# Kernel tuning notes

Measured on AMD Instinct MI355X. Metric: run time of the kernel, lower is better.

The kernel has to match this reference:

```python
import jax, jax.numpy as jnp
import numpy as np

B, C, T, H, W, L = 4, 256, 8, 16, 16, 8
NO = 8                # num_offsets
D = C // NO           # per-head feature dim for offset/weight MLPs
EPS = 1e-5


def setup_inputs() -> dict:
    key = jax.random.key(0)
    ks = jax.random.split(key, 6)
    return {
        "features": jax.random.normal(ks[0], (B, C, T, H, W, L), jnp.float32),
        "pos": jax.random.normal(ks[1], (B, C, T, H, W, L), jnp.float32),
        "Wp": jax.random.normal(ks[2], (C, 3 * C), jnp.float32) * 0.02,  # 1x1x1 conv: 3C -> C
        "bp": jnp.zeros((C,), jnp.float32),
        "Wo": jax.random.normal(ks[3], (D, 3), jnp.float32) * 0.02,      # offset_embed Linear(d,3)
        "bo": jnp.zeros((3,), jnp.float32),
        "Ww": jax.random.normal(ks[4], (D, 2), jnp.float32) * 0.02,      # weight_embed Linear(d,2)
        "bw": jnp.zeros((2,), jnp.float32),
    }


def _trilinear_sample(feat, coords):
    """feat: (N,C,D1,D2,D3); coords: (N,G,3) in [-1,1] (axis order D1,D2,D3).
    align_corners=False, zeros padding (matches F.grid_sample semantics)."""
    N, Cc, D1, D2, D3 = feat.shape
    sizes = jnp.asarray([D1, D2, D3], feat.dtype)
    pix = ((coords + 1.0) * sizes - 1.0) * 0.5       # unnormalize to pixel coords
    lo = jnp.floor(pix)
    frac = pix - lo                                   # (N,G,3)
    lo = lo.astype(jnp.int32)
    dims = jnp.asarray([D1, D2, D3], jnp.int32)
    feat_flat = feat.reshape(N, Cc, D1 * D2 * D3)
    out = jnp.zeros((N, Cc, coords.shape[1]), feat.dtype)
    for dz in (0, 1):
        for dy in (0, 1):
            for dx in (0, 1):
                off = jnp.asarray([dz, dy, dx], jnp.int32)
                idx = lo + off                        # (N,G,3)
                wz = jnp.where(dz, frac[..., 0], 1.0 - frac[..., 0])
                wy = jnp.where(dy, frac[..., 1], 1.0 - frac[..., 1])
                wx = jnp.where(dx, frac[..., 2], 1.0 - frac[..., 2])
                wgt = wz * wy * wx                    # (N,G)
                valid = jnp.all((idx >= 0) & (idx < dims), axis=-1)
                idc = jnp.clip(idx, 0, dims - 1)
                lin = (idc[..., 0] * D2 + idc[..., 1]) * D3 + idc[..., 2]  # (N,G)
                vals = jnp.take_along_axis(feat_flat, lin[:, None, :], axis=2)  # (N,C,G)
                out = out + vals * (wgt * valid)[:, None, :]
    return out


def reference(features, pos, Wp, bp, Wo, bo, Ww, bw):
    Bv, Cv, Tv, Hv, Wv, Lv = features.shape
    BT = Bv * Tv
    feat = features.transpose(0, 2, 1, 3, 4, 5).reshape(BT, Cv, Hv, Wv, Lv)
    posr = pos.transpose(0, 2, 1, 3, 4, 5).reshape(BT, Cv, Hv, Wv, Lv)
    # global context + projection (1x1x1 conv over 3C channels) + ReLU
    glob = feat.mean(axis=(2, 3, 4), keepdims=True)
    src = jnp.concatenate([feat, posr, jnp.broadcast_to(glob, feat.shape)], axis=1)  # (BT,3C,H,W,L)
    proj = jax.nn.relu(jnp.einsum('nixyz,oi->noxyz', src, Wp) + bp[None, :, None, None, None])
    osrc = proj.transpose(0, 2, 3, 4, 1).reshape(BT, Hv, Wv, Lv, NO, D)
    # per-voxel per-head offsets in (0,1) and scalar weights
    offset = jax.nn.sigmoid(osrc @ Wo + bo)                      # (BT,H,W,L,NO,3)
    wgt = jax.nn.softmax(osrc @ Ww + bw, axis=-1)[..., 1]        # (BT,H,W,L,NO)
    # base flow field in [-1,1], deform in logit space, re-sigmoid
    base = jnp.stack(jnp.meshgrid(jnp.linspace(-1.0, 1.0, Hv),
                                  jnp.linspace(-1.0, 1.0, Wv),
                                  jnp.linspace(-1.0, 1.0, Lv), indexing='ij'), axis=-1)
    base01 = jnp.clip((base + 1.0) * 0.5, EPS, 1.0 - EPS)
    logit = jnp.log(base01 / (1.0 - base01))                     # (H,W,L,3)
    sp = jax.nn.sigmoid(logit[None, :, :, :, None, :] + offset)  # (BT,H,W,L,NO,3)
    grid = (sp * 2.0 - 1.0).transpose(0, 4, 1, 2, 3, 5).reshape(BT, NO * Hv * Wv * Lv, 3)
    sampled = _trilinear_sample(feat, grid).reshape(BT, Cv, NO, Hv, Wv, Lv)
    out = feat + jnp.einsum('bcnhwl,bhwln->bchwl', sampled, wgt)
    return out.reshape(Bv, Tv, Cv, Hv, Wv, Lv).transpose(0, 2, 1, 3, 4, 5)
```

## Files before the change

### kernel.cpp

```cpp
#include <hip/hip_runtime.h>

#define BB 4
#define CC 256
#define TT 8
#define HH 16
#define WW 16
#define LL 8
#define NO 8
#define DD 32
#define BT 32
#define VV 2048
#define KIN 512
#define EPS_ 1e-5f

typedef short bf16x8 __attribute__((ext_vector_type(8)));
typedef float f32x4 __attribute__((ext_vector_type(4)));

static __device__ __forceinline__ float b2f(unsigned short u) {
    return __uint_as_float(((unsigned int)u) << 16);
}
static __device__ __forceinline__ float b2f_lo(unsigned int x) {
    return __uint_as_float(x << 16);
}
static __device__ __forceinline__ float b2f_hi(unsigned int x) {
    return __uint_as_float(x & 0xffff0000u);
}
static __device__ __forceinline__ unsigned short f2b(float f) {
    unsigned int x = __float_as_uint(f);
    unsigned int r = x + 0x7fffu + ((x >> 16) & 1u);
    return (unsigned short)(r >> 16);
}
static __device__ __forceinline__ unsigned int f2b_pk(float lo, float hi) {
    return (unsigned int)f2b(lo) | ((unsigned int)f2b(hi) << 16);
}
static __device__ __forceinline__ float sigm(float x) {
    return 1.0f / (1.0f + __expf(-x));
}

__global__ __launch_bounds__(256) void k0_prep(const float* __restrict__ Wp,
                                               unsigned short* __restrict__ Wa,
                                               float* __restrict__ glob) {
    int i = blockIdx.x * 256 + threadIdx.x;
    if (i < CC * KIN) {
        int o = i >> 9, k = i & 511;
        Wa[i] = f2b(Wp[o * 768 + k]);
    } else if (i < CC * KIN + BT * CC) {
        glob[i - CC * KIN] = 0.0f;
    }
}

__global__ __launch_bounds__(256) void k1_transpose(const float* __restrict__ features,
                                                    const float* __restrict__ pos,
                                                    unsigned short* __restrict__ srcT,
                                                    float* __restrict__ glob) {
    const int n = blockIdx.x;
    const int v0 = blockIdx.y * 16;
    const int b = n >> 3, t = n & 7;
    const int tid = threadIdx.x;
    const int ty = tid >> 4;
    const int tx = tid & 15;

    __shared__ unsigned short s1[16 * 520];

    for (int cb = 0; cb < CC; cb += 16) {
        int c = cb + ty;
        size_t fidx = (((size_t)b * CC + c) * TT + t) * VV + v0 + tx;
        float f = features[fidx];
        float p = pos[fidx];
        s1[tx * 520 + c] = f2b(f);
        s1[tx * 520 + 256 + c] = f2b(p);
        for (int d = 8; d > 0; d >>= 1) f += __shfl_down(f, d, 16);
        if (tx == 0) atomicAdd(&glob[n * CC + c], f);
    }
    __syncthreads();
    const size_t base = ((size_t)n * VV + v0) * KIN;
    for (int q = tid; q < 1024; q += 256) {
        int row = q >> 6;
        int koff = (q & 63) * 8;
        *(uint4*)&srcT[base + (size_t)row * KIN + koff] = *(const uint4*)&s1[row * 520 + koff];
    }
}

__global__ __launch_bounds__(256) void k2_gterm(const float* __restrict__ glob,
                                                const float* __restrict__ Wp,
                                                const float* __restrict__ bp,
                                                float* __restrict__ gterm) {
    const int n = blockIdx.x;
    const int o = threadIdx.x;
    __shared__ float gl[CC];
    gl[o] = glob[n * CC + o] * (1.0f / (float)VV);
    __syncthreads();
    const float4* wrow = (const float4*)(Wp + (size_t)o * 768 + 512);
    const float4* g4 = (const float4*)gl;
    float s = bp[o];
    #pragma unroll 8
    for (int c = 0; c < 64; ++c) {
        float4 w = wrow[c], g = g4[c];
        s += w.x * g.x + w.y * g.y + w.z * g.z + w.w * g.w;
    }
    gterm[n * CC + o] = s;
}

__global__ __launch_bounds__(256) void k3_gemm(const unsigned short* __restrict__ Wa,
                                               const unsigned short* __restrict__ srcT,
                                               const float* __restrict__ gterm,
                                               unsigned short* __restrict__ projT) {
    const int n  = blockIdx.x;
    const int mb = blockIdx.y;
    const int nb = blockIdx.z;
    const int tid = threadIdx.x;
    const int m0 = mb * 128, v0 = nb * 128;

    __shared__ short As[128 * 40];
    __shared__ short Bs[128 * 40];

    const int wv = tid >> 6;
    const int lane = tid & 63;
    const int wm = wv >> 1, wn = wv & 1;
    const int lr = lane & 15, lq = lane >> 4;

    f32x4 acc[4][4];
    #pragma unroll
    for (int i = 0; i < 4; ++i)
        #pragma unroll
        for (int j = 0; j < 4; ++j)
            acc[i][j] = (f32x4){0.f, 0.f, 0.f, 0.f};

    const int row = tid >> 1, half = tid & 1;
    const unsigned short* agp = Wa + (size_t)(m0 + row) * KIN + half * 16;
    const unsigned short* bgp = srcT + ((size_t)n * VV + v0 + row) * KIN + half * 16;
    short* asp = &As[row * 40 + half * 16];
    short* bsp = &Bs[row * 40 + half * 16];

    for (int k0 = 0; k0 < KIN; k0 += 32) {
        uint4 a0 = *(const uint4*)(agp + k0);
        uint4 a1 = *(const uint4*)(agp + k0 + 8);
        uint4 b0 = *(const uint4*)(bgp + k0);
        uint4 b1 = *(const uint4*)(bgp + k0 + 8);
        __syncthreads();
        *(uint4*)asp = a0; *(uint4*)(asp + 8) = a1;
        *(uint4*)bsp = b0; *(uint4*)(bsp + 8) = b1;
        __syncthreads();

        bf16x8 af[4], bf[4];
        #pragma unroll
        for (int i = 0; i < 4; ++i)
            af[i] = *(const bf16x8*)&As[(wm * 64 + i * 16 + lr) * 40 + lq * 8];
        #pragma unroll
        for (int j = 0; j < 4; ++j)
            bf[j] = *(const bf16x8*)&Bs[(wn * 64 + j * 16 + lr) * 40 + lq * 8];
        #pragma unroll
        for (int i = 0; i < 4; ++i)
            #pragma unroll
            for (int j = 0; j < 4; ++j)
                acc[i][j] = __builtin_amdgcn_mfma_f32_16x16x32_bf16(af[i], bf[j], acc[i][j], 0, 0, 0);
    }

    #pragma unroll
    for (int i = 0; i < 4; ++i) {
        const int og = m0 + wm * 64 + i * 16 + lq * 4;
        float4 g = *(const float4*)(gterm + n * CC + og);
        #pragma unroll
        for (int j = 0; j < 4; ++j) {
            const int vg = v0 + wn * 64 + j * 16 + lr;
            float x0 = fmaxf(acc[i][j][0] + g.x, 0.0f);
            float x1 = fmaxf(acc[i][j][1] + g.y, 0.0f);
            float x2 = fmaxf(acc[i][j][2] + g.z, 0.0f);
            float x3 = fmaxf(acc[i][j][3] + g.w, 0.0f);
            ushort4 st;
            st.x = f2b(x0); st.y = f2b(x1); st.z = f2b(x2); st.w = f2b(x3);
            *(ushort4*)&projT[((size_t)n * VV + vg) * CC + og] = st;
        }
    }
}

__global__ __launch_bounds__(256) void k4_coef(const unsigned short* __restrict__ projT,
                                               const float* __restrict__ Wo,
                                               const float* __restrict__ bo,
                                               const float* __restrict__ Ww,
                                               const float* __restrict__ bw,
                                               int2* __restrict__ pairs) {
    __shared__ float sWo[96], sWw[64], sb[5];
    const int tid = threadIdx.x;
    if (tid < 96) sWo[tid] = Wo[tid];
    if (tid < 64) sWw[tid] = Ww[tid];
    if (tid < 3)  sb[tid] = bo[tid];
    if (tid < 2)  sb[3 + tid] = bw[tid];
    __syncthreads();

    const int g = blockIdx.x * 256 + tid;
    const int n = g >> 14;
    const int rem = g & 16383;
    const int v = rem >> 3;
    const int hd = rem & 7;

    const uint4* up = (const uint4*)(projT + ((size_t)n * VV + v) * CC + hd * DD);
    float osrc[32];
    #pragma unroll
    for (int q = 0; q < 4; ++q) {
        uint4 u = up[q];
        unsigned int ws4[4] = {u.x, u.y, u.z, u.w};
        #pragma unroll
        for (int e = 0; e < 4; ++e) {
            osrc[q * 8 + e * 2]     = b2f_lo(ws4[e]);
            osrc[q * 8 + e * 2 + 1] = b2f_hi(ws4[e]);
        }
    }

    float o0 = sb[0], o1 = sb[1], o2 = sb[2];
    float zw = sb[4] - sb[3];
    #pragma unroll
    for (int d = 0; d < DD; ++d) {
        float t = osrc[d];
        o0 += t * sWo[3 * d + 0];
        o1 += t * sWo[3 * d + 1];
        o2 += t * sWo[3 * d + 2];
        zw += t * (sWw[2 * d + 1] - sWw[2 * d]);
    }
    const float wgt = sigm(zw);

    const int h = v >> 7, w = (v >> 3) & 15, l = v & 7;
    float ph = fminf(fmaxf(h * (1.0f / 15.0f), EPS_), 1.0f - EPS_);
    float pw = fminf(fmaxf(w * (1.0f / 15.0f), EPS_), 1.0f - EPS_);
    float pl = fminf(fmaxf(l * (1.0f / 7.0f),  EPS_), 1.0f - EPS_);
    float lh = __logf(ph / (1.0f - ph));
    float lw = __logf(pw / (1.0f - pw));
    float ll = __logf(pl / (1.0f - pl));

    float sph = sigm(lh + sigm(o0));
    float spw = sigm(lw + sigm(o1));
    float spl = sigm(ll + sigm(o2));
    float pixh = sph * 16.0f - 0.5f;
    float pixw = spw * 16.0f - 0.5f;
    float pixl = spl * 8.0f  - 0.5f;

    float flh = floorf(pixh), flw = floorf(pixw), fll = floorf(pixl);
    float fh = pixh - flh, fw = pixw - flw, fl = pixl - fll;
    int ih = (int)flh, iw = (int)flw, il = (int)fll;

    int2* pp = pairs + (size_t)g * 8;
    #pragma unroll
    for (int dz = 0; dz < 2; ++dz)
        #pragma unroll
        for (int dy = 0; dy < 2; ++dy)
            #pragma unroll
            for (int dx = 0; dx < 2; ++dx) {
                int iz = ih + dz, iy = iw + dy, ix = il + dx;
                float wt = (dz ? fh : 1.0f - fh) * (dy ? fw : 1.0f - fw) * (dx ? fl : 1.0f - fl) * wgt;
                bool valid = ((unsigned)iz < 16u) && ((unsigned)iy < 16u) && ((unsigned)ix < 8u);
                int lin = valid ? ((iz * 16 + iy) * 8 + ix) : 0;
                float wv2 = valid ? wt : 0.0f;
                pp[dz * 4 + dy * 2 + dx] = make_int2(lin, __float_as_int(wv2));
            }
}

__global__ __launch_bounds__(256) void k5_gather(const unsigned short* __restrict__ srcT,
                                                 const int2* __restrict__ pairs,
                                                 unsigned short* __restrict__ res) {
    __shared__ int2 pr[8 * 64];
    const int n  = blockIdx.x >> 8;
    const int vb = (blockIdx.x & 255) * 8;
    const int tid = threadIdx.x;

    {
        const int2* src = pairs + ((size_t)n * VV + vb) * 64;
        *(int4*)&pr[tid * 2] = *(const int4*)&src[tid * 2];
    }
    __syncthreads();

    const int s = tid >> 5;
    const int lane = tid & 31;
    const int c8 = lane * 8;
    const unsigned short* slab = srcT + (size_t)n * VV * KIN + c8;
    const int2* pe = &pr[s * 64];

    float a0 = 0.f, a1 = 0.f, a2 = 0.f, a3 = 0.f;
    float a4 = 0.f, a5 = 0.f, a6 = 0.f, a7 = 0.f;

    #pragma unroll 1
    for (int e = 0; e < 64; e += 8) {
        uint4 f[8];
        float w[8];
        #pragma unroll
        for (int u = 0; u < 8; ++u) {
            int2 q = pe[e + u];
            w[u] = __int_as_float(q.y);
            f[u] = *(const uint4*)(slab + (size_t)q.x * KIN);
        }
        #pragma unroll
        for (int u = 0; u < 8; ++u) {
            a0 = fmaf(w[u], b2f_lo(f[u].x), a0);
            a1 = fmaf(w[u], b2f_hi(f[u].x), a1);
            a2 = fmaf(w[u], b2f_lo(f[u].y), a2);
            a3 = fmaf(w[u], b2f_hi(f[u].y), a3);
            a4 = fmaf(w[u], b2f_lo(f[u].z), a4);
            a5 = fmaf(w[u], b2f_hi(f[u].z), a5);
            a6 = fmaf(w[u], b2f_lo(f[u].w), a6);
            a7 = fmaf(w[u], b2f_hi(f[u].w), a7);
        }
    }

    uint4 st;
    st.x = f2b_pk(a0, a1);
    st.y = f2b_pk(a2, a3);
    st.z = f2b_pk(a4, a5);
    st.w = f2b_pk(a6, a7);
    *(uint4*)&res[((size_t)n * VV + vb + s) * CC + c8] = st;
}

__global__ __launch_bounds__(256) void k6_final(const float* __restrict__ features,
                                                const unsigned short* __restrict__ res,
                                                float* __restrict__ out) {
    const int n = blockIdx.x;
    const int c0 = blockIdx.y * 64;
    const int v0 = blockIdx.z * 64;
    const int b = n >> 3, t = n & 7;
    const int tid = threadIdx.x;
    const int ty = tid >> 6, tx = tid & 63;

    __shared__ unsigned short t6[64 * 66];

    for (int vv = ty; vv < 64; vv += 4)
        t6[vv * 66 + tx] = res[((size_t)n * VV + v0 + vv) * CC + c0 + tx];
    __syncthreads();
    for (int cc = ty; cc < 64; cc += 4) {
        int c = c0 + cc;
        size_t oidx = (((size_t)b * CC + c) * TT + t) * VV + v0 + tx;
        out[oidx] = features[oidx] + b2f(t6[tx * 66 + cc]);
    }
}

extern "C" void kernel_launch(void* const* d_in, const int* in_sizes, int n_in,
                              void* d_out, int out_size, void* d_ws, size_t ws_size,
                              hipStream_t stream) {
    (void)in_sizes; (void)n_in; (void)out_size; (void)ws_size;
    const float* features = (const float*)d_in[0];
    const float* pos      = (const float*)d_in[1];
    const float* Wp       = (const float*)d_in[2];
    const float* bp       = (const float*)d_in[3];
    const float* Wo       = (const float*)d_in[4];
    const float* bo       = (const float*)d_in[5];
    const float* Ww       = (const float*)d_in[6];
    const float* bw       = (const float*)d_in[7];
    float* out = (float*)d_out;

    char* ws = (char*)d_ws;
    unsigned short* srcT  = (unsigned short*)ws;
    unsigned short* Wa    = (unsigned short*)(ws + 67108864);
    float*          glob  = (float*)(ws + 67371008);
    float*          gterm = (float*)(ws + 67403776);
    unsigned short* projT = (unsigned short*)(ws + 67436544);
    int2*           pairs = (int2*)(ws + 100990976);
    unsigned short* res   = projT;

    k0_prep<<<544, 256, 0, stream>>>(Wp, Wa, glob);
    k1_transpose<<<dim3(32, 128), 256, 0, stream>>>(features, pos, srcT, glob);
    k2_gterm<<<32, 256, 0, stream>>>(glob, Wp, bp, gterm);
    k3_gemm<<<dim3(32, 2, 16), 256, 0, stream>>>(Wa, srcT, gterm, projT);
    k4_coef<<<2048, 256, 0, stream>>>(projT, Wo, bo, Ww, bw, pairs);
    k5_gather<<<8192, 256, 0, stream>>>(srcT, pairs, res);
    k6_final<<<dim3(32, 4, 32), 256, 0, stream>>>(features, res, out);
}
```

Before: 361.5 us.

## Replace global-mean atomics with partial sums; vectorize gather FMAs and byte offsets

The global channel sums were built with atomicAdd into a zeroed buffer. They are now written as per-tile partial sums into a scratch area that aliases the pairs buffer, and k2 reduces them, so the zeroing in k0 and the atomic contention go away. The gather kernel now gets precomputed byte offsets (row index shifted by 10) and uses packed two-wide FMAs, which should cut address arithmetic and VALU instruction count. The cost is an extra 4MB partial-sum write and read, plus k2 doing a 128-step serial reduction.

```diff
diff --git a/kernel.cpp b/kernel.cpp
--- a/kernel.cpp
+++ b/kernel.cpp
@@ -15,6 +15,7 @@
 
 typedef short bf16x8 __attribute__((ext_vector_type(8)));
 typedef float f32x4 __attribute__((ext_vector_type(4)));
+typedef float f32x2 __attribute__((ext_vector_type(2)));
 
 static __device__ __forceinline__ float b2f(unsigned short u) {
     return __uint_as_float(((unsigned int)u) << 16);
@@ -38,23 +39,19 @@
 }
 
 __global__ __launch_bounds__(256) void k0_prep(const float* __restrict__ Wp,
-                                               unsigned short* __restrict__ Wa,
-                                               float* __restrict__ glob) {
+                                               unsigned short* __restrict__ Wa) {
     int i = blockIdx.x * 256 + threadIdx.x;
-    if (i < CC * KIN) {
-        int o = i >> 9, k = i & 511;
-        Wa[i] = f2b(Wp[o * 768 + k]);
-    } else if (i < CC * KIN + BT * CC) {
-        glob[i - CC * KIN] = 0.0f;
-    }
+    int o = i >> 9, k = i & 511;
+    Wa[i] = f2b(Wp[o * 768 + k]);
 }
 
 __global__ __launch_bounds__(256) void k1_transpose(const float* __restrict__ features,
                                                     const float* __restrict__ pos,
                                                     unsigned short* __restrict__ srcT,
-                                                    float* __restrict__ glob) {
+                                                    float* __restrict__ gpart) {
     const int n = blockIdx.x;
-    const int v0 = blockIdx.y * 16;
+    const int vt = blockIdx.y;
+    const int v0 = vt * 16;
     const int b = n >> 3, t = n & 7;
     const int tid = threadIdx.x;
     const int ty = tid >> 4;
@@ -70,7 +67,7 @@
         s1[tx * 520 + c] = f2b(f);
         s1[tx * 520 + 256 + c] = f2b(p);
         for (int d = 8; d > 0; d >>= 1) f += __shfl_down(f, d, 16);
-        if (tx == 0) atomicAdd(&glob[n * CC + c], f);
+        if (tx == 0) gpart[((size_t)n * 128 + vt) * CC + c] = f;
     }
     __syncthreads();
     const size_t base = ((size_t)n * VV + v0) * KIN;
@@ -81,24 +78,28 @@
     }
 }
 
-__global__ __launch_bounds__(256) void k2_gterm(const float* __restrict__ glob,
+__global__ __launch_bounds__(256) void k2_gterm(const float* __restrict__ gpart,
                                                 const float* __restrict__ Wp,
                                                 const float* __restrict__ bp,
                                                 float* __restrict__ gterm) {
     const int n = blockIdx.x;
     const int o = threadIdx.x;
     __shared__ float gl[CC];
-    gl[o] = glob[n * CC + o] * (1.0f / (float)VV);
+    float s = 0.0f;
+    const float* gp = gpart + (size_t)n * 128 * CC + o;
+    #pragma unroll 8
+    for (int vt = 0; vt < 128; ++vt) s += gp[(size_t)vt * CC];
+    gl[o] = s * (1.0f / (float)VV);
     __syncthreads();
     const float4* wrow = (const float4*)(Wp + (size_t)o * 768 + 512);
     const float4* g4 = (const float4*)gl;
-    float s = bp[o];
+    float acc = bp[o];
     #pragma unroll 8
     for (int c = 0; c < 64; ++c) {
         float4 w = wrow[c], g = g4[c];
-        s += w.x * g.x + w.y * g.y + w.z * g.z + w.w * g.w;
-    }
-    gterm[n * CC + o] = s;
+        acc += w.x * g.x + w.y * g.y + w.z * g.z + w.w * g.w;
+    }
+    gterm[n * CC + o] = acc;
 }
 
 __global__ __launch_bounds__(256) void k3_gemm(const unsigned short* __restrict__ Wa,
@@ -248,7 +249,7 @@
                 int iz = ih + dz, iy = iw + dy, ix = il + dx;
                 float wt = (dz ? fh : 1.0f - fh) * (dy ? fw : 1.0f - fw) * (dx ? fl : 1.0f - fl) * wgt;
                 bool valid = ((unsigned)iz < 16u) && ((unsigned)iy < 16u) && ((unsigned)ix < 8u);
-                int lin = valid ? ((iz * 16 + iy) * 8 + ix) : 0;
+                int lin = valid ? (((iz * 16 + iy) * 8 + ix) << 10) : 0;
                 float wv2 = valid ? wt : 0.0f;
                 pp[dz * 4 + dy * 2 + dx] = make_int2(lin, __float_as_int(wv2));
             }
@@ -270,12 +271,11 @@
 
     const int s = tid >> 5;
     const int lane = tid & 31;
-    const int c8 = lane * 8;
-    const unsigned short* slab = srcT + (size_t)n * VV * KIN + c8;
+    const unsigned int laneoff = (unsigned int)lane * 16u;
+    const char* slabB = (const char*)srcT + (size_t)n * VV * KIN * 2;
     const int2* pe = &pr[s * 64];
 
-    float a0 = 0.f, a1 = 0.f, a2 = 0.f, a3 = 0.f;
-    float a4 = 0.f, a5 = 0.f, a6 = 0.f, a7 = 0.f;
+    f32x2 a0 = {0.f, 0.f}, a1 = {0.f, 0.f}, a2 = {0.f, 0.f}, a3 = {0.f, 0.f};
 
     #pragma unroll 1
     for (int e = 0; e < 64; e += 8) {
@@ -285,27 +285,28 @@
         for (int u = 0; u < 8; ++u) {
             int2 q = pe[e + u];
             w[u] = __int_as_float(q.y);
-            f[u] = *(const uint4*)(slab + (size_t)q.x * KIN);
+            f[u] = *(const uint4*)(slabB + ((unsigned int)q.x + laneoff));
         }
         #pragma unroll
         for (int u = 0; u < 8; ++u) {
-            a0 = fmaf(w[u], b2f_lo(f[u].x), a0);
-            a1 = fmaf(w[u], b2f_hi(f[u].x), a1);
-            a2 = fmaf(w[u], b2f_lo(f[u].y), a2);
-            a3 = fmaf(w[u], b2f_hi(f[u].y), a3);
-            a4 = fmaf(w[u], b2f_lo(f[u].z), a4);
-            a5 = fmaf(w[u], b2f_hi(f[u].z), a5);
-            a6 = fmaf(w[u], b2f_lo(f[u].w), a6);
-            a7 = fmaf(w[u], b2f_hi(f[u].w), a7);
+            f32x2 w2 = {w[u], w[u]};
+            f32x2 t0 = {b2f_lo(f[u].x), b2f_hi(f[u].x)};
+            f32x2 t1 = {b2f_lo(f[u].y), b2f_hi(f[u].y)};
+            f32x2 t2 = {b2f_lo(f[u].z), b2f_hi(f[u].z)};
+            f32x2 t3 = {b2f_lo(f[u].w), b2f_hi(f[u].w)};
+            a0 = __builtin_elementwise_fma(w2, t0, a0);
+            a1 = __builtin_elementwise_fma(w2, t1, a1);
+            a2 = __builtin_elementwise_fma(w2, t2, a2);
+            a3 = __builtin_elementwise_fma(w2, t3, a3);
         }
     }
 
     uint4 st;
-    st.x = f2b_pk(a0, a1);
-    st.y = f2b_pk(a2, a3);
-    st.z = f2b_pk(a4, a5);
-    st.w = f2b_pk(a6, a7);
-    *(uint4*)&res[((size_t)n * VV + vb + s) * CC + c8] = st;
+    st.x = f2b_pk(a0.x, a0.y);
+    st.y = f2b_pk(a1.x, a1.y);
+    st.z = f2b_pk(a2.x, a2.y);
+    st.w = f2b_pk(a3.x, a3.y);
+    *(uint4*)&res[((size_t)n * VV + vb + s) * CC + lane * 8] = st;
 }
 
 __global__ __launch_bounds__(256) void k6_final(const float* __restrict__ features,
@@ -347,15 +348,15 @@
     char* ws = (char*)d_ws;
     unsigned short* srcT  = (unsigned short*)ws;
     unsigned short* Wa    = (unsigned short*)(ws + 67108864);
-    float*          glob  = (float*)(ws + 67371008);
     float*          gterm = (float*)(ws + 67403776);
     unsigned short* projT = (unsigned short*)(ws + 67436544);
     int2*           pairs = (int2*)(ws + 100990976);
+    float*          gpart = (float*)(ws + 100990976);
     unsigned short* res   = projT;
 
-    k0_prep<<<544, 256, 0, stream>>>(Wp, Wa, glob);
-    k1_transpose<<<dim3(32, 128), 256, 0, stream>>>(features, pos, srcT, glob);
-    k2_gterm<<<32, 256, 0, stream>>>(glob, Wp, bp, gterm);
+    k0_prep<<<512, 256, 0, stream>>>(Wp, Wa);
+    k1_transpose<<<dim3(32, 128), 256, 0, stream>>>(features, pos, srcT, gpart);
+    k2_gterm<<<32, 256, 0, stream>>>(gpart, Wp, bp, gterm);
     k3_gemm<<<dim3(32, 2, 16), 256, 0, stream>>>(Wa, srcT, gterm, projT);
     k4_coef<<<2048, 256, 0, stream>>>(projT, Wo, bo, Ww, bw, pairs);
     k5_gather<<<8192, 256, 0, stream>>>(srcT, pairs, res);
```

Result: slower. 373.3 us (+3.3%).
